# Optimization experiments

Hardware: AMD Instinct MI355X
Metric: run time of the kernel (lower is better)

## Reference

```python
import jax, jax.numpy as jnp
import numpy as np
from jax import lax


def _conv(x, w, b, pad):
    # x: [B,C,H,W], w: [O,I,kh,kw]
    y = lax.conv_general_dilated(x, w, (1, 1), [(pad, pad), (pad, pad)],
                                 dimension_numbers=('NCHW', 'OIHW', 'NCHW'))
    return y + b[None, :, None, None]


def _maxpool2(x):
    return lax.reduce_window(x, -jnp.inf, lax.max, (1, 1, 2, 2), (1, 1, 2, 2), 'VALID')


def setup_inputs() -> dict:
    key = jax.random.key(0)
    ks = jax.random.split(key, 6)
    N, T, R, D = 8, 64, 9, 512
    x = jax.random.normal(ks[0], (N, T, R, D), dtype=jnp.float32)
    x = x / jnp.linalg.norm(x, axis=-1, keepdims=True)  # ViSiL features are L2-normalized
    w1 = jax.random.normal(ks[1], (32, 1, 3, 3), dtype=jnp.float32) * 0.05
    w2 = jax.random.normal(ks[2], (64, 32, 3, 3), dtype=jnp.float32) * 0.05
    w3 = jax.random.normal(ks[3], (128, 64, 3, 3), dtype=jnp.float32) * 0.05
    w4 = jax.random.normal(ks[4], (1, 128, 1, 1), dtype=jnp.float32) * 0.05
    return {
        'x': x,
        'w1': w1, 'b1': jnp.zeros((32,), jnp.float32),
        'w2': w2, 'b2': jnp.zeros((64,), jnp.float32),
        'w3': w3, 'b3': jnp.zeros((128,), jnp.float32),
        'w4': w4, 'b4': jnp.zeros((1,), jnp.float32),
    }


def reference(x, w1, b1, w2, b2, w3, b3, w4, b4):
    N, T, R, D = x.shape
    # frame-to-frame similarity: region correlation volume + chamfer (max over p, mean over o)
    sim = jnp.einsum('aiok,bjpk->aiopjb', x, x)        # [a,i,o,p,j,b]
    sim = jnp.mean(jnp.max(sim, axis=3), axis=2)        # [a,i,j,b]
    sim = jnp.transpose(sim, (0, 3, 1, 2)).reshape(N * N, 1, T, T)  # '(a b) () i j'
    # VideoComparator CNN head (ZeroPad2d(1) + valid 3x3 conv == 'same' 3x3 conv)
    h = jax.nn.relu(_conv(sim, w1, b1, 1))
    h = _maxpool2(h)
    h = jax.nn.relu(_conv(h, w2, b2, 1))
    h = _maxpool2(h)
    h = jax.nn.relu(_conv(h, w3, b3, 1))
    h = _conv(h, w4, b4, 0)                              # [N*N, 1, T/4, T/4]
    # SimilarityRegularizationLoss(min_val=-1, max_val=1)
    loss = jnp.sum(jax.nn.relu(-(h + 1.0))) + jnp.sum(jax.nn.relu(h - 1.0))
    # Hardtanh, rescale to [0,1], then video-to-video chamfer
    s = jnp.clip(h, -1.0, 1.0) / 2.0 + 0.5
    s = jnp.mean(jnp.max(s, axis=3), axis=2)             # [N*N, 1]
    return s.reshape(N, N), loss
```

## Files before the change

### kernel.cpp

```cpp
#include <hip/hip_runtime.h>

typedef unsigned short u16;
typedef unsigned int u32;
typedef __bf16 bf16x8 __attribute__((ext_vector_type(8)));
typedef u16 u16x8 __attribute__((ext_vector_type(8)));
typedef float f32x4 __attribute__((ext_vector_type(4)));

__device__ __forceinline__ u16 f2bf(float f) {
  u32 u = __float_as_uint(f);
  u32 r = (u + 0x7FFFu + ((u >> 16) & 1u)) >> 16;
  return (u16)r;
}

__device__ __forceinline__ void gload16(const void* g, void* l) {
  typedef __attribute__((address_space(1))) const void gvoid;
  typedef __attribute__((address_space(3))) void lvoid;
  __builtin_amdgcn_global_load_lds((gvoid*)g, (lvoid*)l, 16, 0, 0);
}

__global__ void k_cast(const float* __restrict__ x, u16* __restrict__ A,
                       const float* __restrict__ w2, const float* __restrict__ w3,
                       u16* __restrict__ p2, u16* __restrict__ p3,
                       float* __restrict__ out) {
  int t = blockIdx.x * 256 + threadIdx.x;
  const float4* xp = (const float4*)x + (size_t)t * 2;
  float4 v0 = xp[0], v1 = xp[1];
  u16x8 r;
  r[0] = f2bf(v0.x); r[1] = f2bf(v0.y); r[2] = f2bf(v0.z); r[3] = f2bf(v0.w);
  r[4] = f2bf(v1.x); r[5] = f2bf(v1.y); r[6] = f2bf(v1.z); r[7] = f2bf(v1.w);
  *(u16x8*)(A + (size_t)t * 8) = r;
  if (blockIdx.x == 0 && threadIdx.x < 65) out[threadIdx.x] = 0.f;
  if (t < 18432) {
    int tt = t >> 11, oc = (t >> 5) & 63, ic = t & 31;
    p2[t] = f2bf(w2[(oc * 32 + ic) * 9 + tt]);
  }
  if (t < 73728) {
    int tt = t >> 13, oc = (t >> 6) & 127, ic = t & 63;
    p3[t] = f2bf(w3[(oc * 64 + ic) * 9 + tt]);
  }
}

__global__ __launch_bounds__(256) void k_gemm_smax(const u16* __restrict__ A,
                                                   float* __restrict__ Smax,
                                                   float* __restrict__ Sx) {
  __shared__ char smem[65536];
  float* slab = (float*)smem;
  const int chunk = blockIdx.x & 7, ci = blockIdx.x >> 3;
  const int csz = (chunk < 2) ? 84 : 83;
  if (ci >= csz) return;
  const int tlin = ((chunk < 2) ? 84 * chunk : 168 + 83 * (chunk - 2)) + ci;
  int rb = (int)((73.0f - sqrtf((float)(5329 - 8 * tlin))) * 0.5f);
  while (rb * 36 - rb * (rb - 1) / 2 > tlin) --rb;
  while ((rb + 1) * 36 - (rb + 1) * rb / 2 <= tlin) ++rb;
  const int cb = rb + (tlin - (rb * 36 - rb * (rb - 1) / 2));
  const int rowBase = rb * 128, colBase = cb * 128;
  const int tid = threadIdx.x, wave = tid >> 6, lane = tid & 63;
  const int lr = lane >> 3, lc = lane & 7;
  const int lrow = lane & 15, lk = lane >> 4;
  const int xr = lrow & 7;
  const int wr = (wave & 1) * 64, wc = (wave >> 1) * 64;

  f32x4 acc[4][4];
#pragma unroll
  for (int rt = 0; rt < 4; ++rt)
#pragma unroll
    for (int ct = 0; ct < 4; ++ct) { f32x4 z = {0.f, 0.f, 0.f, 0.f}; acc[rt][ct] = z; }

  {
    u16* As = (u16*)smem;
    u16* Bs = (u16*)(smem + 16384);
#pragma unroll
    for (int ii = 0; ii < 4; ++ii) {
      int r0 = wave * 32 + ii * 8;
      gload16(A + (size_t)(rowBase + r0 + lr) * 512 + ((lc ^ lr) * 8), As + r0 * 64);
      gload16(A + (size_t)(colBase + r0 + lr) * 512 + ((lc ^ lr) * 8), Bs + r0 * 64);
    }
  }
  __syncthreads();
  for (int k = 0; k < 8; ++k) {
    if (k < 7) {
      char* base = smem + (((k + 1) & 1) << 15);
      u16* As = (u16*)base;
      u16* Bs = (u16*)(base + 16384);
      int k0 = (k + 1) * 64;
#pragma unroll
      for (int ii = 0; ii < 4; ++ii) {
        int r0 = wave * 32 + ii * 8;
        gload16(A + (size_t)(rowBase + r0 + lr) * 512 + k0 + ((lc ^ lr) * 8),
                As + r0 * 64);
        gload16(A + (size_t)(colBase + r0 + lr) * 512 + k0 + ((lc ^ lr) * 8),
                Bs + r0 * 64);
      }
    }
    {
      char* base = smem + ((k & 1) << 15);
      u16* As = (u16*)base;
      u16* Bs = (u16*)(base + 16384);
#pragma unroll
      for (int s = 0; s < 2; ++s) {
        bf16x8 af[4], bf[4];
#pragma unroll
        for (int rt = 0; rt < 4; ++rt)
          af[rt] = *(const bf16x8*)(As + (wr + rt * 16 + lrow) * 64 +
                                    ((u32)(s * 4 + lk) ^ xr) * 8);
#pragma unroll
        for (int ct = 0; ct < 4; ++ct)
          bf[ct] = *(const bf16x8*)(Bs + (wc + ct * 16 + lrow) * 64 +
                                    ((u32)(s * 4 + lk) ^ xr) * 8);
#pragma unroll
        for (int rt = 0; rt < 4; ++rt)
#pragma unroll
          for (int ct = 0; ct < 4; ++ct)
            acc[rt][ct] = __builtin_amdgcn_mfma_f32_16x16x32_bf16(af[rt], bf[ct],
                                                                  acc[rt][ct], 0, 0, 0);
      }
    }
    __syncthreads();
  }

  const int g0c = colBase / 9, offc = colBase % 9;
  const int g0r = rowBase / 9, offr = rowBase % 9;
  const int nph = (rb == cb) ? 2 : 4;
  for (int ph = 0; ph < nph; ++ph) {
    __syncthreads();
    if (ph < 2) {
      if ((wave & 1) == ph) {
#pragma unroll
        for (int rt = 0; rt < 4; ++rt)
#pragma unroll
          for (int ct = 0; ct < 4; ++ct)
#pragma unroll
            for (int r = 0; r < 4; ++r)
              slab[(rt * 16 + lk * 4 + r) * 129 + wc + ct * 16 + lrow] = acc[rt][ct][r];
      }
    } else {
      if ((wave >> 1) == ph - 2) {
#pragma unroll
        for (int rt = 0; rt < 4; ++rt)
#pragma unroll
          for (int ct = 0; ct < 4; ++ct)
#pragma unroll
            for (int r = 0; r < 4; ++r)
              slab[(ct * 16 + lrow) * 129 + wr + rt * 16 + lk * 4 + r] = acc[rt][ct][r];
      }
    }
    __syncthreads();
    for (int it = tid; it < 1024; it += 256) {
      int line = it >> 4, s = it & 15;
      float m = -3.0e38f;
      if (ph < 2) {
        int g = g0c + s;
        int cs = 9 * g - colBase, ce = cs + 9;
        cs = cs < 0 ? 0 : cs;
        ce = ce > 128 ? 128 : ce;
        if (cs >= ce) continue;
        const float* p = slab + line * 129;
        for (int c = cs; c < ce; ++c) m = fmaxf(m, p[c]);
        int r = rowBase + ph * 64 + line;
        if (s == 0 && offc != 0) Sx[(size_t)r * 36 + (cb - 1)] = m;
        else Smax[(size_t)r * 512 + g] = m;
      } else {
        int g = g0r + s;
        int rs = 9 * g - rowBase, re = rs + 9;
        rs = rs < 0 ? 0 : rs;
        re = re > 128 ? 128 : re;
        if (rs >= re) continue;
        const float* p = slab + line * 129;
        for (int r2 = rs; r2 < re; ++r2) m = fmaxf(m, p[r2]);
        int cgl = colBase + (ph - 2) * 64 + line;
        if (s == 0 && offr != 0) Sx[(size_t)cgl * 36 + (rb - 1)] = m;
        else Smax[(size_t)cgl * 512 + g] = m;
      }
    }
  }
}

__global__ void k_reduce_o(const float* __restrict__ Smax, const float* __restrict__ Sx,
                           float* __restrict__ sim) {
  int idx = blockIdx.x * 256 + threadIdx.x;
  int j = idx & 63, i = (idx >> 6) & 63, b = (idx >> 12) & 7, a = idx >> 15;
  int g = b * 64 + j;
  int t9 = 9 * g;
  int k = (t9 + 8) >> 7;
  bool part = ((u32)(128 * k - t9 - 1) < 8u);
  const float* p = Smax + (size_t)(a * 576 + i * 9) * 512 + g;
  const float* q = Sx + (size_t)(a * 576 + i * 9) * 36 + (k - 1);
  float s = 0.f;
#pragma unroll
  for (int o = 0; o < 9; ++o) {
    float v = p[o * 512];
    if (part) v = fmaxf(v, q[o * 36]);
    s += v;
  }
  sim[idx] = s * (1.f / 9.f);
}

__global__ __launch_bounds__(256) void k_conv1pool(const float* __restrict__ sim,
                                                   const float* __restrict__ w1,
                                                   const float* __restrict__ b1,
                                                   u16* __restrict__ h1) {
  __shared__ float tin[4096];
  const int pair = blockIdx.x, ocg = blockIdx.y, tid = threadIdx.x;
  const float4* src = (const float4*)(sim + (size_t)pair * 4096);
  for (int i = tid; i < 1024; i += 256) ((float4*)tin)[i] = src[i];
  __syncthreads();
  float wv[8][9], bs[8];
#pragma unroll
  for (int o = 0; o < 8; ++o) {
#pragma unroll
    for (int q = 0; q < 9; ++q) wv[o][q] = w1[(ocg * 8 + o) * 9 + q];
    bs[o] = b1[ocg * 8 + o];
  }
  for (int pp = tid; pp < 1024; pp += 256) {
    int py = pp >> 5, px = pp & 31;
    float m[8];
#pragma unroll
    for (int o = 0; o < 8; ++o) m[o] = 0.f;
#pragma unroll
    for (int dy = 0; dy < 2; ++dy)
#pragma unroll
      for (int dx = 0; dx < 2; ++dx) {
        float s[8];
#pragma unroll
        for (int o = 0; o < 8; ++o) s[o] = bs[o];
        int yy = py * 2 + dy, xx0 = px * 2 + dx;
#pragma unroll
        for (int ky = 0; ky < 3; ++ky) {
          int y = yy + ky - 1;
          if ((unsigned)y < 64u) {
#pragma unroll
            for (int kx = 0; kx < 3; ++kx) {
              int x = xx0 + kx - 1;
              if ((unsigned)x < 64u) {
                float v = tin[y * 64 + x];
#pragma unroll
                for (int o = 0; o < 8; ++o) s[o] += wv[o][ky * 3 + kx] * v;
              }
            }
          }
        }
#pragma unroll
        for (int o = 0; o < 8; ++o) m[o] = fmaxf(m[o], fmaxf(s[o], 0.f));
      }
    u16x8 r;
#pragma unroll
    for (int o = 0; o < 8; ++o) r[o] = f2bf(m[o]);
    *(u16x8*)&h1[(((size_t)pair * 32 + py) * 32 + px) * 32 + ocg * 8] = r;
  }
}

__global__ __launch_bounds__(256) void k_conv2pool(const u16* __restrict__ h1,
                                                   const u16* __restrict__ wp2,
                                                   const float* __restrict__ b2,
                                                   u16* __restrict__ h2) {
  __shared__ u16 tile[18 * 34 * 40];
  const int pair = blockIdx.x, yh = blockIdx.y, tid = threadIdx.x;
  const int wave = tid >> 6, lane = tid & 63, l15 = lane & 15, quad = lane >> 4;
  u16x8 z8 = {0, 0, 0, 0, 0, 0, 0, 0};
  for (int i = tid; i < 3060; i += 256) ((u16x8*)tile)[i] = z8;
  __syncthreads();
  for (int f = tid; f < 1152; f += 256) {
    int i = f >> 6, rem = f & 63, px = rem >> 1, half = rem & 1;
    int gr = yh * 16 - 1 + i;
    if ((unsigned)gr < 32u)
      *(u16x8*)&tile[(i * 34 + 1 + px) * 40 + half * 16] =
          *(const u16x8*)&h1[(((size_t)pair * 32 + gr) * 32 + px) * 32 + half * 16];
  }
  __syncthreads();

  f32x4 acc[8][4];
#pragma unroll
  for (int m = 0; m < 8; ++m)
#pragma unroll
    for (int n = 0; n < 4; ++n) { f32x4 z = {0.f, 0.f, 0.f, 0.f}; acc[m][n] = z; }

  for (int t = 0; t < 9; ++t) {
    int ky = t / 3, kx = t % 3;
    bf16x8 wf[4];
#pragma unroll
    for (int nt = 0; nt < 4; ++nt)
      wf[nt] = *(const bf16x8*)&wp2[((t * 64 + nt * 16 + l15) << 5) + quad * 8];
#pragma unroll
    for (int rr = 0; rr < 4; ++rr)
#pragma unroll
      for (int xh = 0; xh < 2; ++xh) {
        int lr = wave * 4 + rr;
        bf16x8 af = *(const bf16x8*)&tile[((lr + ky) * 34 + xh * 16 + l15 + kx) * 40 +
                                          quad * 8];
#pragma unroll
        for (int nt = 0; nt < 4; ++nt)
          acc[rr * 2 + xh][nt] =
              __builtin_amdgcn_mfma_f32_16x16x32_bf16(af, wf[nt], acc[rr * 2 + xh][nt],
                                                      0, 0, 0);
      }
  }

  float bv[4];
#pragma unroll
  for (int nt = 0; nt < 4; ++nt) bv[nt] = b2[nt * 16 + l15];
#pragma unroll
  for (int rp = 0; rp < 2; ++rp)
#pragma unroll
    for (int xh = 0; xh < 2; ++xh) {
      int py = yh * 8 + wave * 2 + rp;
      int px0 = xh * 8 + quad * 2;
#pragma unroll
      for (int nt = 0; nt < 4; ++nt) {
        f32x4 va = acc[(rp * 2) * 2 + xh][nt], vb = acc[(rp * 2 + 1) * 2 + xh][nt];
        float p0 = fmaxf(fmaxf(fmaxf(va[0], va[1]), fmaxf(vb[0], vb[1])) + bv[nt], 0.f);
        float p1 = fmaxf(fmaxf(fmaxf(va[2], va[3]), fmaxf(vb[2], vb[3])) + bv[nt], 0.f);
        size_t base = (((size_t)pair * 16 + py) * 16 + px0) * 64 + nt * 16 + l15;
        h2[base] = f2bf(p0);
        h2[base + 64] = f2bf(p1);
      }
    }
}

__global__ __launch_bounds__(256) void k_conv3(const u16* __restrict__ h2,
                                               const u16* __restrict__ wp3,
                                               const float* __restrict__ b3,
                                               float* __restrict__ h3) {
  __shared__ u16 tile[18 * 18 * 72];
  const int pair = blockIdx.x, oh = blockIdx.y, tid = threadIdx.x;
  const int wave = tid >> 6, lane = tid & 63, l15 = lane & 15, quad = lane >> 4;
  u16x8 z8 = {0, 0, 0, 0, 0, 0, 0, 0};
  for (int i = tid; i < 2916; i += 256) ((u16x8*)tile)[i] = z8;
  __syncthreads();
  for (int f = tid; f < 2048; f += 256) {
    int row = f >> 7, rem = f & 127, px = rem >> 3, seg = rem & 7;
    *(u16x8*)&tile[((row + 1) * 18 + px + 1) * 72 + seg * 8] =
        *(const u16x8*)&h2[(((size_t)pair * 16 + row) * 16 + px) * 64 + seg * 8];
  }
  __syncthreads();

  f32x4 acc[4][4];
#pragma unroll
  for (int m = 0; m < 4; ++m)
#pragma unroll
    for (int n = 0; n < 4; ++n) { f32x4 z = {0.f, 0.f, 0.f, 0.f}; acc[m][n] = z; }

  for (int t = 0; t < 9; ++t) {
    int ky = t / 3, kx = t % 3;
#pragma unroll
    for (int s = 0; s < 2; ++s) {
      bf16x8 wf[4];
#pragma unroll
      for (int nt = 0; nt < 4; ++nt)
        wf[nt] = *(const bf16x8*)&wp3[((t * 128 + oh * 64 + nt * 16 + l15) << 6) +
                                      s * 32 + quad * 8];
#pragma unroll
      for (int yt = 0; yt < 4; ++yt) {
        int y = wave * 4 + yt;
        bf16x8 af = *(const bf16x8*)&tile[((y + ky) * 18 + l15 + kx) * 72 + s * 32 +
                                          quad * 8];
#pragma unroll
        for (int nt = 0; nt < 4; ++nt)
          acc[yt][nt] = __builtin_amdgcn_mfma_f32_16x16x32_bf16(af, wf[nt],
                                                                acc[yt][nt], 0, 0, 0);
      }
    }
  }

  float bv[4];
#pragma unroll
  for (int nt = 0; nt < 4; ++nt) bv[nt] = b3[oh * 64 + nt * 16 + l15];
#pragma unroll
  for (int yt = 0; yt < 4; ++yt)
#pragma unroll
    for (int nt = 0; nt < 4; ++nt)
#pragma unroll
      for (int r = 0; r < 4; ++r) {
        int px = (wave * 4 + yt) * 16 + quad * 4 + r;
        h3[((size_t)pair * 256 + px) * 128 + oh * 64 + nt * 16 + l15] =
            fmaxf(acc[yt][nt][r] + bv[nt], 0.f);
      }
}

__global__ __launch_bounds__(256) void k_conv4(const float* __restrict__ h3,
                                               const float* __restrict__ w4,
                                               const float* __restrict__ b4,
                                               float* __restrict__ out) {
  __shared__ float ws4[128];
  __shared__ float rowmax[16];
  __shared__ float lsum[4];
  const int pair = blockIdx.x, tid = threadIdx.x;
  if (tid < 128) ws4[tid] = w4[tid];
  __syncthreads();
  float h = b4[0];
  const float4* p = (const float4*)(h3 + ((size_t)pair * 256 + tid) * 128);
#pragma unroll 8
  for (int i = 0; i < 32; ++i) {
    float4 v = p[i];
    h += v.x * ws4[i * 4] + v.y * ws4[i * 4 + 1] + v.z * ws4[i * 4 + 2] +
         v.w * ws4[i * 4 + 3];
  }
  float loss = fmaxf(-(h + 1.f), 0.f) + fmaxf(h - 1.f, 0.f);
  float sc = fminf(fmaxf(h, -1.f), 1.f) * 0.5f + 0.5f;
#pragma unroll
  for (int off = 8; off >= 1; off >>= 1) sc = fmaxf(sc, __shfl_xor(sc, off, 16));
#pragma unroll
  for (int off = 32; off >= 1; off >>= 1) loss += __shfl_xor(loss, off, 64);
  if ((tid & 15) == 0) rowmax[tid >> 4] = sc;
  if ((tid & 63) == 0) lsum[tid >> 6] = loss;
  __syncthreads();
  if (tid == 0) {
    float mean = 0.f;
#pragma unroll
    for (int i = 0; i < 16; ++i) mean += rowmax[i];
    out[pair] = mean * (1.f / 16.f);
    atomicAdd(out + 64, lsum[0] + lsum[1] + lsum[2] + lsum[3]);
  }
}

extern "C" void kernel_launch(void* const* d_in, const int* in_sizes, int n_in,
                              void* d_out, int out_size, void* d_ws, size_t ws_size,
                              hipStream_t stream) {
  (void)in_sizes; (void)n_in; (void)out_size; (void)ws_size;
  const float* x  = (const float*)d_in[0];
  const float* w1 = (const float*)d_in[1];
  const float* b1 = (const float*)d_in[2];
  const float* w2 = (const float*)d_in[3];
  const float* b2 = (const float*)d_in[4];
  const float* w3 = (const float*)d_in[5];
  const float* b3 = (const float*)d_in[6];
  const float* w4 = (const float*)d_in[7];
  const float* b4 = (const float*)d_in[8];
  float* out = (float*)d_out;

  char* ws = (char*)d_ws;
  u16*   Abf  = (u16*)ws;
  float* Smax = (float*)(ws + 4718592);
  float* Sx   = (float*)(ws + 14155776);
  float* sim  = (float*)(ws + 14819328);
  u16*   h1   = (u16*)(ws + 15867904);
  u16*   h2   = (u16*)(ws + 20062208);
  float* h3   = (float*)(ws + 22159360);
  u16*   wp2  = (u16*)(ws + 30547968);
  u16*   wp3  = (u16*)(ws + 30584832);

  k_cast<<<1152, 256, 0, stream>>>(x, Abf, w2, w3, wp2, wp3, out);
  k_gemm_smax<<<672, 256, 0, stream>>>(Abf, Smax, Sx);
  k_reduce_o<<<1024, 256, 0, stream>>>(Smax, Sx, sim);
  k_conv1pool<<<dim3(64, 4), 256, 0, stream>>>(sim, w1, b1, h1);
  k_conv2pool<<<dim3(64, 2), 256, 0, stream>>>(h1, wp2, b2, h2);
  k_conv3<<<dim3(64, 2), 256, 0, stream>>>(h2, wp3, b3, h3);
  k_conv4<<<64, 256, 0, stream>>>(h3, w4, b4, out);
}
```

Measured before the change: 159.2 us.

## Fuse conv3 and 1x1 conv4 with loss/chamfer epilogue into one kernel

Merges the 3x3 conv3 and the 1x1 conv4 head into a single kernel. Each block now computes all 128 output channels for one pair and applies bias, ReLU and the w4 dot product in registers. The 1x1 conv is reduced with lane shuffles, and the hardtanh row-max and regularization loss are computed in the same epilogue. This removes the fp32 h3 intermediate round trip through global memory and one kernel launch. In exchange the grid halves to 64 blocks and each thread holds twice as many accumulators, which lowers parallelism and raises register pressure.

```diff
diff --git a/kernel.cpp b/kernel.cpp
--- a/kernel.cpp
+++ b/kernel.cpp
@@ -316,12 +316,16 @@
     }
 }
 
-__global__ __launch_bounds__(256) void k_conv3(const u16* __restrict__ h2,
-                                               const u16* __restrict__ wp3,
-                                               const float* __restrict__ b3,
-                                               float* __restrict__ h3) {
+__global__ __launch_bounds__(256) void k_conv34(const u16* __restrict__ h2,
+                                                const u16* __restrict__ wp3,
+                                                const float* __restrict__ b3,
+                                                const float* __restrict__ w4,
+                                                const float* __restrict__ b4,
+                                                float* __restrict__ out) {
   __shared__ u16 tile[18 * 18 * 72];
-  const int pair = blockIdx.x, oh = blockIdx.y, tid = threadIdx.x;
+  __shared__ float lrow[16];
+  __shared__ float lsw[4];
+  const int pair = blockIdx.x, tid = threadIdx.x;
   const int wave = tid >> 6, lane = tid & 63, l15 = lane & 15, quad = lane >> 4;
   u16x8 z8 = {0, 0, 0, 0, 0, 0, 0, 0};
   for (int i = tid; i < 2916; i += 256) ((u16x8*)tile)[i] = z8;
@@ -333,82 +337,77 @@
   }
   __syncthreads();
 
-  f32x4 acc[4][4];
+  f32x4 acc[4][8];
 #pragma unroll
   for (int m = 0; m < 4; ++m)
 #pragma unroll
-    for (int n = 0; n < 4; ++n) { f32x4 z = {0.f, 0.f, 0.f, 0.f}; acc[m][n] = z; }
+    for (int n = 0; n < 8; ++n) { f32x4 z = {0.f, 0.f, 0.f, 0.f}; acc[m][n] = z; }
 
   for (int t = 0; t < 9; ++t) {
     int ky = t / 3, kx = t % 3;
 #pragma unroll
     for (int s = 0; s < 2; ++s) {
-      bf16x8 wf[4];
-#pragma unroll
-      for (int nt = 0; nt < 4; ++nt)
-        wf[nt] = *(const bf16x8*)&wp3[((t * 128 + oh * 64 + nt * 16 + l15) << 6) +
-                                      s * 32 + quad * 8];
+      bf16x8 wf[8];
+#pragma unroll
+      for (int nt = 0; nt < 8; ++nt)
+        wf[nt] = *(const bf16x8*)&wp3[((t * 128 + nt * 16 + l15) << 6) + s * 32 +
+                                      quad * 8];
 #pragma unroll
       for (int yt = 0; yt < 4; ++yt) {
         int y = wave * 4 + yt;
         bf16x8 af = *(const bf16x8*)&tile[((y + ky) * 18 + l15 + kx) * 72 + s * 32 +
                                           quad * 8];
 #pragma unroll
-        for (int nt = 0; nt < 4; ++nt)
+        for (int nt = 0; nt < 8; ++nt)
           acc[yt][nt] = __builtin_amdgcn_mfma_f32_16x16x32_bf16(af, wf[nt],
                                                                 acc[yt][nt], 0, 0, 0);
       }
     }
   }
 
-  float bv[4];
-#pragma unroll
-  for (int nt = 0; nt < 4; ++nt) bv[nt] = b3[oh * 64 + nt * 16 + l15];
-#pragma unroll
-  for (int yt = 0; yt < 4; ++yt)
-#pragma unroll
-    for (int nt = 0; nt < 4; ++nt)
-#pragma unroll
-      for (int r = 0; r < 4; ++r) {
-        int px = (wave * 4 + yt) * 16 + quad * 4 + r;
-        h3[((size_t)pair * 256 + px) * 128 + oh * 64 + nt * 16 + l15] =
-            fmaxf(acc[yt][nt][r] + bv[nt], 0.f);
-      }
-}
-
-__global__ __launch_bounds__(256) void k_conv4(const float* __restrict__ h3,
-                                               const float* __restrict__ w4,
-                                               const float* __restrict__ b4,
-                                               float* __restrict__ out) {
-  __shared__ float ws4[128];
-  __shared__ float rowmax[16];
-  __shared__ float lsum[4];
-  const int pair = blockIdx.x, tid = threadIdx.x;
-  if (tid < 128) ws4[tid] = w4[tid];
-  __syncthreads();
-  float h = b4[0];
-  const float4* p = (const float4*)(h3 + ((size_t)pair * 256 + tid) * 128);
-#pragma unroll 8
-  for (int i = 0; i < 32; ++i) {
-    float4 v = p[i];
-    h += v.x * ws4[i * 4] + v.y * ws4[i * 4 + 1] + v.z * ws4[i * 4 + 2] +
-         v.w * ws4[i * 4 + 3];
-  }
-  float loss = fmaxf(-(h + 1.f), 0.f) + fmaxf(h - 1.f, 0.f);
-  float sc = fminf(fmaxf(h, -1.f), 1.f) * 0.5f + 0.5f;
-#pragma unroll
-  for (int off = 8; off >= 1; off >>= 1) sc = fmaxf(sc, __shfl_xor(sc, off, 16));
-#pragma unroll
-  for (int off = 32; off >= 1; off >>= 1) loss += __shfl_xor(loss, off, 64);
-  if ((tid & 15) == 0) rowmax[tid >> 4] = sc;
-  if ((tid & 63) == 0) lsum[tid >> 6] = loss;
+  float w4r[8], bvv[8];
+#pragma unroll
+  for (int nt = 0; nt < 8; ++nt) {
+    w4r[nt] = w4[nt * 16 + l15];
+    bvv[nt] = b3[nt * 16 + l15];
+  }
+  float b4v = b4[0];
+  float lossacc = 0.f;
+#pragma unroll
+  for (int yt = 0; yt < 4; ++yt) {
+    float hp[4] = {0.f, 0.f, 0.f, 0.f};
+#pragma unroll
+    for (int nt = 0; nt < 8; ++nt)
+#pragma unroll
+      for (int r = 0; r < 4; ++r)
+        hp[r] += w4r[nt] * fmaxf(acc[yt][nt][r] + bvv[nt], 0.f);
+#pragma unroll
+    for (int off = 1; off <= 8; off <<= 1)
+#pragma unroll
+      for (int r = 0; r < 4; ++r) hp[r] += __shfl_xor(hp[r], off, 16);
+    float rmax = 0.f, lw = 0.f;
+#pragma unroll
+    for (int r = 0; r < 4; ++r) {
+      float h = hp[r] + b4v;
+      lw += fmaxf(-(h + 1.f), 0.f) + fmaxf(h - 1.f, 0.f);
+      float sc = fminf(fmaxf(h, -1.f), 1.f) * 0.5f + 0.5f;
+      rmax = fmaxf(rmax, sc);
+    }
+    rmax = fmaxf(rmax, __shfl_xor(rmax, 16));
+    rmax = fmaxf(rmax, __shfl_xor(rmax, 32));
+    if (lane == 0) lrow[wave * 4 + yt] = rmax;
+    lossacc += lw;
+  }
+#pragma unroll
+  for (int off = 32; off >= 1; off >>= 1) lossacc += __shfl_xor(lossacc, off);
+  if (lane == 0) lsw[wave] = lossacc * (1.f / 16.f);
   __syncthreads();
   if (tid == 0) {
     float mean = 0.f;
 #pragma unroll
-    for (int i = 0; i < 16; ++i) mean += rowmax[i];
+    for (int i = 0; i < 16; ++i) mean += lrow[i];
     out[pair] = mean * (1.f / 16.f);
-    atomicAdd(out + 64, lsum[0] + lsum[1] + lsum[2] + lsum[3]);
+    atomicAdd(out + 64, lsw[0] + lsw[1] + lsw[2] + lsw[3]);
   }
 }
 
@@ -434,15 +433,13 @@
   float* sim  = (float*)(ws + 14819328);
   u16*   h1   = (u16*)(ws + 15867904);
   u16*   h2   = (u16*)(ws + 20062208);
-  float* h3   = (float*)(ws + 22159360);
-  u16*   wp2  = (u16*)(ws + 30547968);
-  u16*   wp3  = (u16*)(ws + 30584832);
+  u16*   wp2  = (u16*)(ws + 22159360);
+  u16*   wp3  = (u16*)(ws + 22196224);
 
   k_cast<<<1152, 256, 0, stream>>>(x, Abf, w2, w3, wp2, wp3, out);
   k_gemm_smax<<<672, 256, 0, stream>>>(Abf, Smax, Sx);
   k_reduce_o<<<1024, 256, 0, stream>>>(Smax, Sx, sim);
   k_conv1pool<<<dim3(64, 4), 256, 0, stream>>>(sim, w1, b1, h1);
   k_conv2pool<<<dim3(64, 2), 256, 0, stream>>>(h1, wp2, b2, h2);
-  k_conv3<<<dim3(64, 2), 256, 0, stream>>>(h2, wp3, b3, h3);
-  k_conv4<<<64, 256, 0, stream>>>(h3, w4, b4, out);
-}
+  k_conv34<<<64, 256, 0, stream>>>(h2, wp3, b3, w4, b4, out);
+}
```

Result: no change. 161.9 us (+1.7%).
